# Kernel tuning notes

Measured on AMD Instinct MI355X. Metric: run time of the kernel, lower is better.

Reference implementation:

```python
import jax, jax.numpy as jnp
import numpy as np

N_NODES = 100000
N_EDGES = 3200000


def gcn_conv(x, src, dst, W, b, n_nodes):
    # PyG GCNConv with default add_self_loops=True, symmetric normalization.
    # src/dst already include self-loops. deg computed on destination.
    ones = jnp.ones(src.shape[0], dtype=x.dtype)
    deg = jax.ops.segment_sum(ones, dst, num_segments=n_nodes)
    dinv = jnp.where(deg > 0, jax.lax.rsqrt(deg), 0.0).astype(x.dtype)
    norm = dinv[src] * dinv[dst]                      # [E]
    h = x @ W                                         # linear first (PyG order)
    msg = h[src] * norm[:, None]                      # gather + scale
    out = jax.ops.segment_sum(msg, dst, num_segments=n_nodes)  # scatter-add
    return out + b


def setup_inputs() -> dict:
    key = jax.random.key(0)
    k1, k2, k3, k4 = jax.random.split(key, 4)
    x = jax.random.normal(k1, (N_NODES, 4), dtype=jnp.float32)
    edge_index = jax.random.randint(k2, (2, N_EDGES), 0, N_NODES, dtype=jnp.int64)
    W1 = jax.random.normal(k3, (4, 32), dtype=jnp.float32) * 0.5
    b1 = jnp.zeros((32,), dtype=jnp.float32)
    W2 = jax.random.normal(k4, (32, 1), dtype=jnp.float32) * 0.2
    b2 = jnp.zeros((1,), dtype=jnp.float32)
    return {"x": x, "edge_index": edge_index, "W1": W1, "b1": b1, "W2": W2, "b2": b2}


def reference(x, edge_index, W1, b1, W2, b2):
    n = x.shape[0]
    # add self-loops once; same augmented graph used by both convs
    loops = jnp.arange(n, dtype=edge_index.dtype)
    src = jnp.concatenate([edge_index[0], loops])
    dst = jnp.concatenate([edge_index[1], loops])
    h = jax.nn.relu(gcn_conv(x, src, dst, W1, b1, n))
    out = jax.nn.sigmoid(gcn_conv(h, src, dst, W2, b2, n))
    return out.squeeze(-1)  # [N] anomaly probability
```

## Files before the change

kernel.cpp:

```cpp
#include <hip/hip_runtime.h>
#include <math.h>
#include <stdint.h>


#define BINBITS 8
#define BINSZ   256
#define NBMAX   512
#define EBC     256
#define THR     256
#define QS      2097152.0f
#define SENT    0xFFFFFFFFu

__device__ __forceinline__ uint32_t packq(float v) {
    return __float2uint_rn(fmaf(v, QS, 16.0f * QS));
}


__global__ void countK(const int* __restrict__ dst, uint32_t* __restrict__ bc,
                       int e, int nb) {
    __shared__ uint32_t cnt[NBMAX];
    int t = threadIdx.x, b = blockIdx.x;
    for (int i = t; i < nb; i += THR) cnt[i] = 0;
    __syncthreads();
    int epb = (e + EBC - 1) / EBC;
    int lo = b * epb, hi = min(e, lo + epb);
    if (((lo | hi) & 3) == 0 && (((uintptr_t)dst & 15) == 0)) {
        const int4* dst4 = (const int4*)dst;
        for (int i = lo / 4 + t; i < hi / 4; i += THR) {
            int4 v = dst4[i];
            atomicAdd(&cnt[((unsigned)v.x) >> BINBITS], 1u);
            atomicAdd(&cnt[((unsigned)v.y) >> BINBITS], 1u);
            atomicAdd(&cnt[((unsigned)v.z) >> BINBITS], 1u);
            atomicAdd(&cnt[((unsigned)v.w) >> BINBITS], 1u);
        }
    } else {
        for (int i = lo + t; i < hi; i += THR)
            atomicAdd(&cnt[((unsigned)dst[i]) >> BINBITS], 1u);
    }
    __syncthreads();
    for (int i = t; i < nb; i += THR) bc[(size_t)i * EBC + b] = cnt[i];
}

__global__ void scan1K(uint32_t* __restrict__ bc, uint32_t* __restrict__ binSum) {
    __shared__ uint32_t s[EBC];
    int t = threadIdx.x, bin = blockIdx.x;
    uint32_t v = bc[(size_t)bin * EBC + t];
    s[t] = v;
    __syncthreads();
    for (int off = 1; off < EBC; off <<= 1) {
        uint32_t u = (t >= off) ? s[t - off] : 0u;
        __syncthreads();
        s[t] += u;
        __syncthreads();
    }
    bc[(size_t)bin * EBC + t] = s[t] - v;
    if (t == EBC - 1) binSum[bin] = s[t];
}

__global__ void scan2K(const uint32_t* __restrict__ binSum,
                       uint32_t* __restrict__ binStart,
                       uint32_t* __restrict__ records, int nb) {
    __shared__ uint32_t s[512];
    int t = threadIdx.x;
    uint32_t real = (t < nb) ? binSum[t] : 0u;
    uint32_t v = (real + 3u) & ~3u;
    s[t] = v;
    __syncthreads();
    for (int off = 1; off < 512; off <<= 1) {
        uint32_t u = (t >= off) ? s[t - off] : 0u;
        __syncthreads();
        s[t] += u;
        __syncthreads();
    }
    if (t < nb) {
        uint32_t start = s[t] - v;
        binStart[t] = start;
        for (uint32_t q = start + real; q < start + v; ++q) records[q] = SENT;
    }
    if (t == nb - 1) binStart[nb] = s[t];
}

__global__ void fillK(const int* __restrict__ src, const int* __restrict__ dst,
                      const uint32_t* __restrict__ bc,
                      const uint32_t* __restrict__ binStart,
                      uint32_t* __restrict__ records, int e, int nb) {
    __shared__ uint32_t cur[NBMAX];
    int t = threadIdx.x;
    int b = (blockIdx.x & 7) * (EBC / 8) + (blockIdx.x >> 3);
    for (int i = t; i < nb; i += THR)
        cur[i] = bc[(size_t)i * EBC + b] + binStart[i];
    __syncthreads();
    int epb = (e + EBC - 1) / EBC;
    int lo = b * epb, hi = min(e, lo + epb);
    if (((lo | hi) & 3) == 0 && (((uintptr_t)src & 15) == 0) && (((uintptr_t)dst & 15) == 0)) {
        const int4* src4 = (const int4*)src;
        const int4* dst4 = (const int4*)dst;
        for (int i = lo / 4 + t; i < hi / 4; i += THR) {
            int4 dv = dst4[i];
            int4 sv = src4[i];
            unsigned d0 = (unsigned)dv.x, d1 = (unsigned)dv.y;
            unsigned d2 = (unsigned)dv.z, d3 = (unsigned)dv.w;
            uint32_t p0 = atomicAdd(&cur[d0 >> BINBITS], 1u);
            records[p0] = (((unsigned)sv.x) << BINBITS) | (d0 & (BINSZ - 1));
            uint32_t p1 = atomicAdd(&cur[d1 >> BINBITS], 1u);
            records[p1] = (((unsigned)sv.y) << BINBITS) | (d1 & (BINSZ - 1));
            uint32_t p2 = atomicAdd(&cur[d2 >> BINBITS], 1u);
            records[p2] = (((unsigned)sv.z) << BINBITS) | (d2 & (BINSZ - 1));
            uint32_t p3 = atomicAdd(&cur[d3 >> BINBITS], 1u);
            records[p3] = (((unsigned)sv.w) << BINBITS) | (d3 & (BINSZ - 1));
        }
    } else {
        for (int i = lo + t; i < hi; i += THR) {
            unsigned d = (unsigned)dst[i];
            unsigned s = (unsigned)src[i];
            uint32_t slot = atomicAdd(&cur[d >> BINBITS], 1u);
            records[slot] = (s << BINBITS) | (d & (BINSZ - 1));
        }
    }
}


__global__ __launch_bounds__(1024)
void degInline(const uint32_t* __restrict__ records,
               const uint32_t* __restrict__ binStart,
               const float4* __restrict__ x4,
               float* __restrict__ dinv, uint32_t* __restrict__ deg,
               ulonglong2* __restrict__ y4q, int n) {
    __shared__ uint32_t hist[BINSZ];
    int t = threadIdx.x, bin = blockIdx.x;
    if (t < BINSZ) hist[t] = 0u;
    __syncthreads();
    uint32_t lo = binStart[bin], hi = binStart[bin + 1];
    const uint4* rec4 = (const uint4*)records;
    for (uint32_t i = lo / 4 + t; i < hi / 4; i += 1024) {
        uint4 r = rec4[i];
        if (r.x != SENT) atomicAdd(&hist[r.x & (BINSZ - 1)], 1u);
        if (r.y != SENT) atomicAdd(&hist[r.y & (BINSZ - 1)], 1u);
        if (r.z != SENT) atomicAdd(&hist[r.z & (BINSZ - 1)], 1u);
        if (r.w != SENT) atomicAdd(&hist[r.w & (BINSZ - 1)], 1u);
    }
    __syncthreads();
    if (t >= BINSZ) return;
    int node = (bin << BINBITS) + t;
    if (node >= n) return;
    uint32_t c = hist[t];
    float dd = rsqrtf(1.0f + (float)c);
    dinv[node] = dd;
    deg[node] = c;
    float4 xv = x4[node];
    uint32_t q0 = packq(dd * xv.x), q1 = packq(dd * xv.y);
    uint32_t q2 = packq(dd * xv.z), q3 = packq(dd * xv.w);
    ulonglong2 p;
    p.x = ((unsigned long long)q1 << 32) | q0;
    p.y = ((unsigned long long)q3 << 32) | q2;
    y4q[node] = p;
}


__global__ void agg_part(const uint32_t* __restrict__ records,
                         const uint32_t* __restrict__ binStart,
                         const ulonglong2* __restrict__ y4q,
                         unsigned long long* __restrict__ aggP, int split) {
    __shared__ unsigned long long acc[2 * BINSZ];
    int t = threadIdx.x;
    int bin = blockIdx.x / split, sub = blockIdx.x % split;
    acc[t] = 0ull;
    acc[BINSZ + t] = 0ull;
    __syncthreads();
    uint32_t lo = binStart[bin], hi = binStart[bin + 1];
    uint32_t chunk = (((hi - lo + split - 1) / split) + 3u) & ~3u;
    uint32_t slo = lo + sub * chunk;
    uint32_t shi = min(hi, slo + chunk);
    const uint4* rec4 = (const uint4*)records;
    for (uint32_t i = slo / 4 + t; i < shi / 4; i += THR) {
        uint4 r = rec4[i];
        unsigned s0 = (r.x == SENT) ? 0u : (r.x >> BINBITS);
        unsigned s1 = (r.y == SENT) ? 0u : (r.y >> BINBITS);
        unsigned s2 = (r.z == SENT) ? 0u : (r.z >> BINBITS);
        unsigned s3 = (r.w == SENT) ? 0u : (r.w >> BINBITS);
        ulonglong2 y0 = y4q[s0];
        ulonglong2 y1 = y4q[s1];
        ulonglong2 y2 = y4q[s2];
        ulonglong2 y3 = y4q[s3];
        if (r.x != SENT) { unsigned d = r.x & (BINSZ - 1); atomicAdd(&acc[d], y0.x); atomicAdd(&acc[BINSZ + d], y0.y); }
        if (r.y != SENT) { unsigned d = r.y & (BINSZ - 1); atomicAdd(&acc[d], y1.x); atomicAdd(&acc[BINSZ + d], y1.y); }
        if (r.z != SENT) { unsigned d = r.z & (BINSZ - 1); atomicAdd(&acc[d], y2.x); atomicAdd(&acc[BINSZ + d], y2.y); }
        if (r.w != SENT) { unsigned d = r.w & (BINSZ - 1); atomicAdd(&acc[d], y3.x); atomicAdd(&acc[BINSZ + d], y3.y); }
    }
    __syncthreads();
    unsigned long long* p = aggP + (size_t)blockIdx.x * (2 * BINSZ);
    p[t] = acc[t];
    p[BINSZ + t] = acc[BINSZ + t];
}

__global__ void mergeAggT(const unsigned long long* __restrict__ aggP,
                          const float* __restrict__ dinv, const uint32_t* __restrict__ deg,
                          const float4* __restrict__ x4,
                          const float* __restrict__ W1, const float* __restrict__ b1,
                          const float* __restrict__ W2,
                          float* __restrict__ g, int split, int n) {
    __shared__ float sW1[128], sb1[32], sW2[32];
    int t = threadIdx.x, bin = blockIdx.x;
    if (t < 128) sW1[t] = W1[t];
    else if (t < 160) sb1[t - 128] = b1[t - 128];
    else if (t < 192) sW2[t - 160] = W2[t - 160];
    __syncthreads();
    int node = (bin << BINBITS) + t;
    if (node >= n) return;
    unsigned long long s0lo = 0, s0hi = 0, s1lo = 0, s1hi = 0;
    size_t base = (size_t)bin * split * (2 * BINSZ);
    for (int s2 = 0; s2 < split; ++s2) {
        const unsigned long long* q = aggP + base + (size_t)s2 * (2 * BINSZ);
        unsigned long long P0 = q[t], P1 = q[BINSZ + t];
        s0lo += (uint32_t)P0; s0hi += (uint32_t)(P0 >> 32);
        s1lo += (uint32_t)P1; s1hi += (uint32_t)(P1 >> 32);
    }
    long long bias = (long long)deg[node] << 25;
    const float inv = 1.0f / QS;
    long long v0 = (long long)s0lo - bias, v1 = (long long)s0hi - bias;
    long long v2 = (long long)s1lo - bias, v3 = (long long)s1hi - bias;
    float T0 = (float)(v0 >> 21) + (float)(v0 & 0x1FFFFF) * inv;
    float T1 = (float)(v1 >> 21) + (float)(v1 & 0x1FFFFF) * inv;
    float T2 = (float)(v2 >> 21) + (float)(v2 & 0x1FFFFF) * inv;
    float T3 = (float)(v3 >> 21) + (float)(v3 & 0x1FFFFF) * inv;
    float dd = dinv[node];
    float4 xv = x4[node];
    float a0 = dd * (T0 + dd * xv.x), a1 = dd * (T1 + dd * xv.y);
    float a2 = dd * (T2 + dd * xv.z), a3 = dd * (T3 + dd * xv.w);
    float hv = 0.f;
#pragma unroll
    for (int j = 0; j < 32; ++j) {
        float o = fmaf(a0, sW1[j], fmaf(a1, sW1[32 + j],
                  fmaf(a2, sW1[64 + j], fmaf(a3, sW1[96 + j], sb1[j]))));
        hv += fmaxf(o, 0.f) * sW2[j];
    }
    g[node] = dd * hv;
}


__global__ __launch_bounds__(1024)
void outInline(const uint32_t* __restrict__ records,
               const uint32_t* __restrict__ binStart,
               const float* __restrict__ g, const float* __restrict__ dinv,
               const float* __restrict__ b2, float* __restrict__ out, int n) {
    __shared__ float accg[BINSZ];
    int t = threadIdx.x, bin = blockIdx.x;
    if (t < BINSZ) accg[t] = 0.f;
    __syncthreads();
    uint32_t lo = binStart[bin], hi = binStart[bin + 1];
    const uint4* rec4 = (const uint4*)records;
    for (uint32_t i = lo / 4 + t; i < hi / 4; i += 1024) {
        uint4 r = rec4[i];
        unsigned s0 = (r.x == SENT) ? 0u : (r.x >> BINBITS);
        unsigned s1 = (r.y == SENT) ? 0u : (r.y >> BINBITS);
        unsigned s2 = (r.z == SENT) ? 0u : (r.z >> BINBITS);
        unsigned s3 = (r.w == SENT) ? 0u : (r.w >> BINBITS);
        float g0 = g[s0], g1 = g[s1], g2 = g[s2], g3 = g[s3];
        if (r.x != SENT) atomicAdd(&accg[r.x & (BINSZ - 1)], g0);
        if (r.y != SENT) atomicAdd(&accg[r.y & (BINSZ - 1)], g1);
        if (r.z != SENT) atomicAdd(&accg[r.z & (BINSZ - 1)], g2);
        if (r.w != SENT) atomicAdd(&accg[r.w & (BINSZ - 1)], g3);
    }
    __syncthreads();
    if (t >= BINSZ) return;
    int node = (bin << BINBITS) + t;
    if (node >= n) return;
    float v = dinv[node] * (accg[t] + g[node]) + b2[0];
    out[node] = 1.0f / (1.0f + expf(-v));
}


extern "C" void kernel_launch(void* const* d_in, const int* in_sizes, int n_in,
                              void* d_out, int out_size, void* d_ws, size_t ws_size,
                              hipStream_t stream) {
    const float* x  = (const float*)d_in[0];
    const int*   ei = (const int*)d_in[1];
    const float* W1 = (const float*)d_in[2];
    const float* b1 = (const float*)d_in[3];
    const float* W2 = (const float*)d_in[4];
    const float* b2 = (const float*)d_in[5];
    float* out = (float*)d_out;

    const int n = in_sizes[0] / 4;
    const int e = in_sizes[1] / 2;
    const int* src = ei;
    const int* dst = ei + e;

    const int nb = (n + BINSZ - 1) >> BINBITS;

    size_t recB  = (((size_t)e + 4 * (size_t)nb) * 4 + 15) & ~(size_t)15;
    size_t bcB   = ((size_t)nb * EBC * 4 + 15) & ~(size_t)15;
    size_t bsB   = ((size_t)(2 * nb + 2) * 4 + 15) & ~(size_t)15;
    size_t dinvB = ((size_t)n * 4 + 15) & ~(size_t)15;
    size_t degB  = ((size_t)n * 4 + 15) & ~(size_t)15;
    size_t gB    = ((size_t)n * 4 + 15) & ~(size_t)15;
    size_t y4qB  = ((size_t)n * 16 + 15) & ~(size_t)15;
    size_t fixed = recB + bcB + bsB + dinvB + degB + gB + y4qB;

    auto arena_sz = [&](int s) { return (size_t)nb * s * (2 * BINSZ) * 8; };

    int split;
    if      (ws_size >= fixed + arena_sz(8)) split = 8;
    else if (ws_size >= fixed + arena_sz(4)) split = 4;
    else if (ws_size >= fixed + arena_sz(2)) split = 2;
    else                                     split = 1;

    char* p = (char*)d_ws;
    uint32_t*   records  = (uint32_t*)p;      p += recB;
    uint32_t*   bc       = (uint32_t*)p;      p += bcB;
    uint32_t*   binStart = (uint32_t*)p;      p += bsB;
    uint32_t*   binSum   = binStart + nb + 1;
    float*      dinv     = (float*)p;         p += dinvB;
    uint32_t*   deg      = (uint32_t*)p;      p += degB;
    float*      gbuf     = (float*)p;         p += gB;
    ulonglong2* y4q      = (ulonglong2*)p;    p += y4qB;
    void*       arena    = (void*)p;

    const float4* x4 = (const float4*)x;

    countK<<<EBC, THR, 0, stream>>>(dst, bc, e, nb);
    scan1K<<<nb, EBC, 0, stream>>>(bc, binSum);
    scan2K<<<1, 512, 0, stream>>>(binSum, binStart, records, nb);
    fillK <<<EBC, THR, 0, stream>>>(src, dst, bc, binStart, records, e, nb);

    degInline<<<nb, 1024, 0, stream>>>(records, binStart, x4, dinv, deg, y4q, n);
    agg_part<<<nb * split, THR, 0, stream>>>(records, binStart, y4q,
                                             (unsigned long long*)arena, split);
    mergeAggT<<<nb, THR, 0, stream>>>((const unsigned long long*)arena, dinv, deg, x4,
                                      W1, b1, W2, gbuf, split, n);
    outInline<<<nb, 1024, 0, stream>>>(records, binStart, gbuf, dinv, b2, out, n);
}
```

Measured before the change: 90.32 us.

## Fuse split aggregation and merge into one 1024-thread block per bin

Replaces the split-partial aggregation kernel and the separate merge/transform kernel with a single kernel that uses one 1024-thread block per destination bin. Each block accumulates all of its bin's records in shared memory, processing two uint4 records per thread per iteration, then directly applies the layer-1 transform. This drops the global partial-sum arena, its write and readback, and one kernel launch. In exchange there are fewer blocks (nb=391) and more threads contending on the same shared-memory atomics per bin.

```diff
diff --git a/kernel.cpp b/kernel.cpp
--- a/kernel.cpp
+++ b/kernel.cpp
@@ -157,64 +157,63 @@
 }
 
 
-__global__ void agg_part(const uint32_t* __restrict__ records,
-                         const uint32_t* __restrict__ binStart,
-                         const ulonglong2* __restrict__ y4q,
-                         unsigned long long* __restrict__ aggP, int split) {
+__global__ __launch_bounds__(1024)
+void aggInline(const uint32_t* __restrict__ records,
+               const uint32_t* __restrict__ binStart,
+               const ulonglong2* __restrict__ y4q,
+               const float* __restrict__ dinv, const uint32_t* __restrict__ deg,
+               const float4* __restrict__ x4,
+               const float* __restrict__ W1, const float* __restrict__ b1,
+               const float* __restrict__ W2,
+               float* __restrict__ g, int n) {
     __shared__ unsigned long long acc[2 * BINSZ];
-    int t = threadIdx.x;
-    int bin = blockIdx.x / split, sub = blockIdx.x % split;
-    acc[t] = 0ull;
-    acc[BINSZ + t] = 0ull;
-    __syncthreads();
-    uint32_t lo = binStart[bin], hi = binStart[bin + 1];
-    uint32_t chunk = (((hi - lo + split - 1) / split) + 3u) & ~3u;
-    uint32_t slo = lo + sub * chunk;
-    uint32_t shi = min(hi, slo + chunk);
-    const uint4* rec4 = (const uint4*)records;
-    for (uint32_t i = slo / 4 + t; i < shi / 4; i += THR) {
-        uint4 r = rec4[i];
-        unsigned s0 = (r.x == SENT) ? 0u : (r.x >> BINBITS);
-        unsigned s1 = (r.y == SENT) ? 0u : (r.y >> BINBITS);
-        unsigned s2 = (r.z == SENT) ? 0u : (r.z >> BINBITS);
-        unsigned s3 = (r.w == SENT) ? 0u : (r.w >> BINBITS);
-        ulonglong2 y0 = y4q[s0];
-        ulonglong2 y1 = y4q[s1];
-        ulonglong2 y2 = y4q[s2];
-        ulonglong2 y3 = y4q[s3];
-        if (r.x != SENT) { unsigned d = r.x & (BINSZ - 1); atomicAdd(&acc[d], y0.x); atomicAdd(&acc[BINSZ + d], y0.y); }
-        if (r.y != SENT) { unsigned d = r.y & (BINSZ - 1); atomicAdd(&acc[d], y1.x); atomicAdd(&acc[BINSZ + d], y1.y); }
-        if (r.z != SENT) { unsigned d = r.z & (BINSZ - 1); atomicAdd(&acc[d], y2.x); atomicAdd(&acc[BINSZ + d], y2.y); }
-        if (r.w != SENT) { unsigned d = r.w & (BINSZ - 1); atomicAdd(&acc[d], y3.x); atomicAdd(&acc[BINSZ + d], y3.y); }
-    }
-    __syncthreads();
-    unsigned long long* p = aggP + (size_t)blockIdx.x * (2 * BINSZ);
-    p[t] = acc[t];
-    p[BINSZ + t] = acc[BINSZ + t];
-}
-
-__global__ void mergeAggT(const unsigned long long* __restrict__ aggP,
-                          const float* __restrict__ dinv, const uint32_t* __restrict__ deg,
-                          const float4* __restrict__ x4,
-                          const float* __restrict__ W1, const float* __restrict__ b1,
-                          const float* __restrict__ W2,
-                          float* __restrict__ g, int split, int n) {
     __shared__ float sW1[128], sb1[32], sW2[32];
     int t = threadIdx.x, bin = blockIdx.x;
-    if (t < 128) sW1[t] = W1[t];
-    else if (t < 160) sb1[t - 128] = b1[t - 128];
-    else if (t < 192) sW2[t - 160] = W2[t - 160];
-    __syncthreads();
+    if (t < 2 * BINSZ) acc[t] = 0ull;
+    else if (t < 2 * BINSZ + 128) sW1[t - 2 * BINSZ] = W1[t - 2 * BINSZ];
+    else if (t < 2 * BINSZ + 160) sb1[t - 2 * BINSZ - 128] = b1[t - 2 * BINSZ - 128];
+    else if (t < 2 * BINSZ + 192) sW2[t - 2 * BINSZ - 160] = W2[t - 2 * BINSZ - 160];
+    __syncthreads();
+    uint32_t base = binStart[bin] / 4, cnt = binStart[bin + 1] / 4;
+    const uint4* rec4 = (const uint4*)records;
+    for (uint32_t i = base + t; i < cnt; i += 2048) {
+        uint4 ra = rec4[i];
+        bool hb = (i + 1024) < cnt;
+        uint4 rb;
+        if (hb) rb = rec4[i + 1024];
+        else    rb = make_uint4(SENT, SENT, SENT, SENT);
+        unsigned a0 = (ra.x == SENT) ? 0u : (ra.x >> BINBITS);
+        unsigned a1 = (ra.y == SENT) ? 0u : (ra.y >> BINBITS);
+        unsigned a2 = (ra.z == SENT) ? 0u : (ra.z >> BINBITS);
+        unsigned a3 = (ra.w == SENT) ? 0u : (ra.w >> BINBITS);
+        unsigned b0 = (rb.x == SENT) ? 0u : (rb.x >> BINBITS);
+        unsigned b1i = (rb.y == SENT) ? 0u : (rb.y >> BINBITS);
+        unsigned b2i = (rb.z == SENT) ? 0u : (rb.z >> BINBITS);
+        unsigned b3 = (rb.w == SENT) ? 0u : (rb.w >> BINBITS);
+        ulonglong2 ya0 = y4q[a0];
+        ulonglong2 ya1 = y4q[a1];
+        ulonglong2 ya2 = y4q[a2];
+        ulonglong2 ya3 = y4q[a3];
+        ulonglong2 yb0 = y4q[b0];
+        ulonglong2 yb1 = y4q[b1i];
+        ulonglong2 yb2 = y4q[b2i];
+        ulonglong2 yb3 = y4q[b3];
+        if (ra.x != SENT) { unsigned d = ra.x & (BINSZ - 1); atomicAdd(&acc[d], ya0.x); atomicAdd(&acc[BINSZ + d], ya0.y); }
+        if (ra.y != SENT) { unsigned d = ra.y & (BINSZ - 1); atomicAdd(&acc[d], ya1.x); atomicAdd(&acc[BINSZ + d], ya1.y); }
+        if (ra.z != SENT) { unsigned d = ra.z & (BINSZ - 1); atomicAdd(&acc[d], ya2.x); atomicAdd(&acc[BINSZ + d], ya2.y); }
+        if (ra.w != SENT) { unsigned d = ra.w & (BINSZ - 1); atomicAdd(&acc[d], ya3.x); atomicAdd(&acc[BINSZ + d], ya3.y); }
+        if (rb.x != SENT) { unsigned d = rb.x & (BINSZ - 1); atomicAdd(&acc[d], yb0.x); atomicAdd(&acc[BINSZ + d], yb0.y); }
+        if (rb.y != SENT) { unsigned d = rb.y & (BINSZ - 1); atomicAdd(&acc[d], yb1.x); atomicAdd(&acc[BINSZ + d], yb1.y); }
+        if (rb.z != SENT) { unsigned d = rb.z & (BINSZ - 1); atomicAdd(&acc[d], yb2.x); atomicAdd(&acc[BINSZ + d], yb2.y); }
+        if (rb.w != SENT) { unsigned d = rb.w & (BINSZ - 1); atomicAdd(&acc[d], yb3.x); atomicAdd(&acc[BINSZ + d], yb3.y); }
+    }
+    __syncthreads();
+    if (t >= BINSZ) return;
     int node = (bin << BINBITS) + t;
     if (node >= n) return;
-    unsigned long long s0lo = 0, s0hi = 0, s1lo = 0, s1hi = 0;
-    size_t base = (size_t)bin * split * (2 * BINSZ);
-    for (int s2 = 0; s2 < split; ++s2) {
-        const unsigned long long* q = aggP + base + (size_t)s2 * (2 * BINSZ);
-        unsigned long long P0 = q[t], P1 = q[BINSZ + t];
-        s0lo += (uint32_t)P0; s0hi += (uint32_t)(P0 >> 32);
-        s1lo += (uint32_t)P1; s1hi += (uint32_t)(P1 >> 32);
-    }
+    unsigned long long P0 = acc[t], P1 = acc[BINSZ + t];
+    unsigned long long s0lo = (uint32_t)P0, s0hi = (uint32_t)(P0 >> 32);
+    unsigned long long s1lo = (uint32_t)P1, s1hi = (uint32_t)(P1 >> 32);
     long long bias = (long long)deg[node] << 25;
     const float inv = 1.0f / QS;
     long long v0 = (long long)s0lo - bias, v1 = (long long)s0hi - bias;
@@ -294,16 +293,6 @@
     size_t dinvB = ((size_t)n * 4 + 15) & ~(size_t)15;
     size_t degB  = ((size_t)n * 4 + 15) & ~(size_t)15;
     size_t gB    = ((size_t)n * 4 + 15) & ~(size_t)15;
-    size_t y4qB  = ((size_t)n * 16 + 15) & ~(size_t)15;
-    size_t fixed = recB + bcB + bsB + dinvB + degB + gB + y4qB;
-
-    auto arena_sz = [&](int s) { return (size_t)nb * s * (2 * BINSZ) * 8; };
-
-    int split;
-    if      (ws_size >= fixed + arena_sz(8)) split = 8;
-    else if (ws_size >= fixed + arena_sz(4)) split = 4;
-    else if (ws_size >= fixed + arena_sz(2)) split = 2;
-    else                                     split = 1;
 
     char* p = (char*)d_ws;
     uint32_t*   records  = (uint32_t*)p;      p += recB;
@@ -313,8 +302,7 @@
     float*      dinv     = (float*)p;         p += dinvB;
     uint32_t*   deg      = (uint32_t*)p;      p += degB;
     float*      gbuf     = (float*)p;         p += gB;
-    ulonglong2* y4q      = (ulonglong2*)p;    p += y4qB;
-    void*       arena    = (void*)p;
+    ulonglong2* y4q      = (ulonglong2*)p;
 
     const float4* x4 = (const float4*)x;
 
@@ -324,9 +312,7 @@
     fillK <<<EBC, THR, 0, stream>>>(src, dst, bc, binStart, records, e, nb);
 
     degInline<<<nb, 1024, 0, stream>>>(records, binStart, x4, dinv, deg, y4q, n);
-    agg_part<<<nb * split, THR, 0, stream>>>(records, binStart, y4q,
-                                             (unsigned long long*)arena, split);
-    mergeAggT<<<nb, THR, 0, stream>>>((const unsigned long long*)arena, dinv, deg, x4,
-                                      W1, b1, W2, gbuf, split, n);
+    aggInline<<<nb, 1024, 0, stream>>>(records, binStart, y4q, dinv, deg, x4,
+                                       W1, b1, W2, gbuf, n);
     outInline<<<nb, 1024, 0, stream>>>(records, binStart, gbuf, dinv, b2, out, n);
 }
```

Result: faster. 83.79 us (-7.2%).
